# Kernel optimization log

Hardware: AMD Instinct MI355X
Metric: run time of the kernel (lower is better)

## Reference

```python
import jax, jax.numpy as jnp
import numpy as np
from jax import lax

B, T, D = 4, 4096, 1024  # d_inner == D (expansion=1.0)


def setup_inputs() -> dict:
    key = jax.random.key(0)
    ks = jax.random.split(key, 6)
    s = 1.0 / np.sqrt(D)  # xavier-ish scale
    return {
        "x": jax.random.normal(ks[0], (B, T, D), dtype=jnp.float32),
        "W_in": jax.random.normal(ks[1], (D, D), dtype=jnp.float32) * s,
        "W_alpha": jax.random.normal(ks[2], (D, D), dtype=jnp.float32) * s,
        "b_alpha": jnp.full((D,), 2.0, dtype=jnp.float32),
        "W_beta": jax.random.normal(ks[3], (D, D), dtype=jnp.float32) * s,
        "b_beta": jnp.zeros((D,), dtype=jnp.float32),
        "W_v": jax.random.normal(ks[4], (D, D), dtype=jnp.float32) * s,
        "b_v": jnp.zeros((D,), dtype=jnp.float32),
        "W_out": jax.random.normal(ks[5], (D, D), dtype=jnp.float32) * s,
    }


def reference(x, W_in, W_alpha, b_alpha, W_beta, b_beta, W_v, b_v, W_out):
    # x: [B, T, D]; torch nn.Linear convention y = x @ W.T
    xp = jax.nn.silu(jnp.einsum("btd,ed->bte", x, W_in))  # [B, T, Di]
    alpha = jax.nn.sigmoid(jnp.einsum("bte,fe->btf", xp, W_alpha) + b_alpha)
    beta = jax.nn.sigmoid(jnp.einsum("bte,fe->btf", xp, W_beta) + b_beta)
    v = jnp.tanh(jnp.einsum("bte,fe->btf", xp, W_v) + b_v)
    bv = beta * v  # precompute write term

    def step(h, ab):
        a_t, bv_t = ab  # each [B, Di]
        h = a_t * h + bv_t
        return h, h * jax.nn.silu(h)

    h0 = jnp.zeros((x.shape[0], W_alpha.shape[0]), dtype=x.dtype)
    h_last, outs = lax.scan(step, h0, (alpha.transpose(1, 0, 2), bv.transpose(1, 0, 2)))
    cell_out = outs.transpose(1, 0, 2)  # [B, T, Di]
    output = jnp.einsum("btf,df->btd", cell_out, W_out)
    return output, h_last
```

## Files before the change

### kernel.cpp

```cpp
#include <hip/hip_runtime.h>
#include <hip/hip_bf16.h>
#include <cstdint>
#include <cstddef>

typedef __bf16 bf16_t;
typedef _Float16 f16_t;
typedef __bf16 bf16x8 __attribute__((ext_vector_type(8)));
typedef float  f32x4  __attribute__((ext_vector_type(4)));

constexpr int kBatch = 4;
constexpr int kT = 4096;
constexpr int kD = 1024;
constexpr int kM = kBatch * kT;
constexpr int kCH = kBatch * kD;
constexpr int kNC = 128;
constexpr int kL  = kT / kNC;
constexpr int LDS_BYTES = 131072;

__device__ __forceinline__ void async16(const bf16_t* g, char* l) {
    __builtin_amdgcn_global_load_lds(
        (const __attribute__((address_space(1))) uint32_t*)g,
        (__attribute__((address_space(3))) uint32_t*)l,
        16, 0, 0);
}

__global__ void cvt_bf16_kernel(const float* __restrict__ in, bf16_t* __restrict__ out, int n8) {
    int i = blockIdx.x * blockDim.x + threadIdx.x;
    if (i >= n8) return;
    const float4* p = reinterpret_cast<const float4*>(in) + 2 * (size_t)i;
    float4 a = p[0], b = p[1];
    bf16x8 o;
    o[0] = (bf16_t)a.x; o[1] = (bf16_t)a.y; o[2] = (bf16_t)a.z; o[3] = (bf16_t)a.w;
    o[4] = (bf16_t)b.x; o[5] = (bf16_t)b.y; o[6] = (bf16_t)b.z; o[7] = (bf16_t)b.w;
    *reinterpret_cast<bf16x8*>(out + 8 * (size_t)i) = o;
}

__global__ void cvtw_kernel(const float* __restrict__ w0, const float* __restrict__ w1,
                            const float* __restrict__ w2, const float* __restrict__ w3,
                            const float* __restrict__ w4, bf16_t* __restrict__ out) {
    const int per = kD * kD / 8;
    int i = blockIdx.x * blockDim.x + threadIdx.x;
    int seg = i / per, j = i - seg * per;
    const float* src = seg == 0 ? w0 : seg == 1 ? w1 : seg == 2 ? w2 : seg == 3 ? w3 : w4;
    const float4* p = reinterpret_cast<const float4*>(src) + 2 * (size_t)j;
    float4 a = p[0], b = p[1];
    bf16x8 o;
    o[0] = (bf16_t)a.x; o[1] = (bf16_t)a.y; o[2] = (bf16_t)a.z; o[3] = (bf16_t)a.w;
    o[4] = (bf16_t)b.x; o[5] = (bf16_t)b.y; o[6] = (bf16_t)b.z; o[7] = (bf16_t)b.w;
    *reinterpret_cast<bf16x8*>(out + ((size_t)seg * per + j) * 8) = o;
}

template<int EPI>
__global__ __launch_bounds__(512, 2)
void gemm256(const bf16_t* __restrict__ A, const bf16_t* __restrict__ Bw,
             const float* __restrict__ bi0, const float* __restrict__ bi1,
             const float* __restrict__ bi2,
             void* __restrict__ out0, void* __restrict__ out1, void* __restrict__ out2,
             int M, int N, int K)
{
    extern __shared__ char lds[];
    const int tid  = threadIdx.x;
    const int lane = tid & 63;
    const int wv   = tid >> 6;
    const int wr   = wv >> 2;
    const int wc   = wv & 3;
    const int l16  = lane & 15;
    const int lhi  = lane >> 4;

    int bid = blockIdx.y * gridDim.x + blockIdx.x;
    int nwg = gridDim.x * gridDim.y;
    int swz = (bid & 7) * (nwg >> 3) + (bid >> 3);
    int gx  = N >> 8;
    int n0  = (swz % gx) << 8;
    int m0  = (swz / gx) << 8;

    auto goff = [&](int chunk) -> size_t {
        int st = chunk >> 6;
        int ri = (chunk >> 2) & 15;
        int cp = (chunk & 3) << 3;
        int cl = cp ^ (((ri >> 3) & 1) << 4);
        int gr = ((st >> 1) << 4) + ri;
        int gc = ((st & 1) << 5) + cl;
        return (size_t)gr * K + gc;
    };
    const size_t g0 = goff(tid), g1 = goff(512 + tid);
    const int d0 = wv << 10, d1 = 8192 + (wv << 10);

    auto STAGE = [&](const bf16_t* G, int row0, int k0, int lds_base) {
        const bf16_t* base = G + (size_t)row0 * K + k0;
        async16(base + g0, lds + lds_base + d0);
        async16(base + g1, lds + lds_base + d1);
    };
    auto STAGE_TILE = [&](int w, int bufo) {
        const int k0 = w << 6;
        STAGE(A,  m0,        k0, bufo);
        STAGE(A,  m0 + 128,  k0, bufo + 16384);
        STAGE(Bw, n0,        k0, bufo + 32768);
        STAGE(Bw, n0 + 128,  k0, bufo + 49152);
    };

    auto ldsoff = [&](int r, int c) -> int {
        int ri = r & 15;
        int st = ((r >> 4) << 1) | (c >> 5);
        int cw = (c & 31) ^ (((ri >> 3) & 1) << 4);
        return (st << 10) + (ri << 6) + (cw << 1);
    };
    int offA[4][2], offB[2][2];
#pragma unroll
    for (int m = 0; m < 4; ++m)
#pragma unroll
        for (int s = 0; s < 2; ++s)
            offA[m][s] = ldsoff(wr * 64 + m * 16 + l16, s * 32 + lhi * 8);
#pragma unroll
    for (int n = 0; n < 2; ++n)
#pragma unroll
        for (int s = 0; s < 2; ++s)
            offB[n][s] = ldsoff(wc * 32 + n * 16 + l16, s * 32 + lhi * 8);

    f32x4 acc[8][4];
#pragma unroll
    for (int i = 0; i < 8; ++i)
#pragma unroll
        for (int j = 0; j < 4; ++j)
            acc[i][j] = (f32x4){0.f, 0.f, 0.f, 0.f};

    const int NT = K >> 6;

    STAGE_TILE(0, 0);
    asm volatile("s_waitcnt vmcnt(0)" ::: "memory");
    asm volatile("s_barrier" ::: "memory");

    for (int w = 0; w < NT; ++w) {
        const int bufo  = (w & 1) << 16;
        const int nbufo = bufo ^ 65536;
        const int oA0 = bufo, oA1 = bufo + 16384;
        const int oB0 = bufo + 32768, oB1 = bufo + 49152;

        if (w + 1 < NT) STAGE_TILE(w + 1, nbufo);

#pragma unroll
        for (int s = 0; s < 2; ++s) {
            bf16x8 aL[4], aH[4], bL[2], bH[2];
#pragma unroll
            for (int m = 0; m < 4; ++m)
                aL[m] = *reinterpret_cast<const bf16x8*>(lds + oA0 + offA[m][s]);
#pragma unroll
            for (int n = 0; n < 2; ++n) {
                bL[n] = *reinterpret_cast<const bf16x8*>(lds + oB0 + offB[n][s]);
                bH[n] = *reinterpret_cast<const bf16x8*>(lds + oB1 + offB[n][s]);
            }
            __builtin_amdgcn_s_setprio(1);
#pragma unroll
            for (int m = 0; m < 4; ++m)
#pragma unroll
                for (int n = 0; n < 2; ++n) {
                    acc[m][n]     = __builtin_amdgcn_mfma_f32_16x16x32_bf16(aL[m], bL[n], acc[m][n], 0, 0, 0);
                    acc[m][2 + n] = __builtin_amdgcn_mfma_f32_16x16x32_bf16(aL[m], bH[n], acc[m][2 + n], 0, 0, 0);
                }
            __builtin_amdgcn_s_setprio(0);
#pragma unroll
            for (int m = 0; m < 4; ++m)
                aH[m] = *reinterpret_cast<const bf16x8*>(lds + oA1 + offA[m][s]);
            __builtin_amdgcn_s_setprio(1);
#pragma unroll
            for (int m = 0; m < 4; ++m)
#pragma unroll
                for (int n = 0; n < 2; ++n) {
                    acc[4 + m][n]     = __builtin_amdgcn_mfma_f32_16x16x32_bf16(aH[m], bL[n], acc[4 + m][n], 0, 0, 0);
                    acc[4 + m][2 + n] = __builtin_amdgcn_mfma_f32_16x16x32_bf16(aH[m], bH[n], acc[4 + m][2 + n], 0, 0, 0);
                }
            __builtin_amdgcn_s_setprio(0);
        }

        if (w + 1 < NT) {
            asm volatile("s_waitcnt vmcnt(0)" ::: "memory");
            asm volatile("s_barrier" ::: "memory");
        }
    }

    const int slab = n0 >> 10;
    const float* bia = (EPI == 4) ? (slab == 0 ? bi0 : slab == 1 ? bi1 : bi2) : nullptr;
#pragma unroll
    for (int j = 0; j < 4; ++j) {
        const int colg = n0 + ((j >> 1) << 7) + wc * 32 + (j & 1) * 16 + l16;
        const int cL = colg & (kD - 1);
        float bs = 0.f;
        if constexpr (EPI == 4) bs = bia[cL];
#pragma unroll
        for (int i = 0; i < 8; ++i) {
            const int rb = m0 + ((i >> 2) << 7) + wr * 64 + (i & 3) * 16 + lhi * 4;
#pragma unroll
            for (int r = 0; r < 4; ++r) {
                const int rowg = rb + r;
                const float f = acc[i][j][r];
                if constexpr (EPI == 0) {
                    float s = f / (1.f + __expf(-f));
                    reinterpret_cast<bf16_t*>(out0)[(size_t)rowg * N + colg] = (bf16_t)s;
                } else if constexpr (EPI == 3) {
                    __builtin_nontemporal_store(f, reinterpret_cast<float*>(out0) + (size_t)rowg * N + colg);
                } else {
                    const size_t idx = (size_t)rowg * kD + cL;
                    if (slab == 0) {
                        float s = 1.f / (1.f + __expf(-(f + bs)));
                        __builtin_nontemporal_store((f16_t)s, reinterpret_cast<f16_t*>(out0) + idx);
                    } else if (slab == 1) {
                        float s = 1.f / (1.f + __expf(-(f + bs)));
                        __builtin_nontemporal_store((bf16_t)s, reinterpret_cast<bf16_t*>(out1) + idx);
                    } else {
                        float s = tanhf(f + bs);
                        __builtin_nontemporal_store((bf16_t)s, reinterpret_cast<bf16_t*>(out2) + idx);
                    }
                }
            }
        }
    }
}

__global__ void scan_chunk_kernel(const f16_t* __restrict__ alpha,
                                  const bf16_t* __restrict__ beta,
                                  const bf16_t* __restrict__ vv,
                                  float* __restrict__ Aagg,
                                  float* __restrict__ Bagg)
{
    const int u  = blockIdx.x * blockDim.x + threadIdx.x;
    const int ch = u & (kCH - 1);
    const int c  = u >> 12;
    const int b  = ch >> 10;
    const int d  = ch & (kD - 1);
    size_t base = ((size_t)b * kT + (size_t)c * kL) * kD + d;
    float Ac = 1.f, Bc = 0.f;
#pragma unroll 4
    for (int t = 0; t < kL; ++t) {
        float a  = (float)alpha[base];
        float bv = (float)beta[base] * (float)vv[base];
        Ac *= a;
        Bc = a * Bc + bv;
        base += kD;
    }
    Aagg[u] = Ac;
    Bagg[u] = Bc;
}

__global__ void scan_mid_kernel(const float* __restrict__ Aagg,
                                const float* __restrict__ Bagg,
                                float* __restrict__ Hin,
                                float* __restrict__ hlast)
{
    const int ch = blockIdx.x * blockDim.x + threadIdx.x;
    float h = 0.f;
#pragma unroll 8
    for (int c = 0; c < kNC; ++c) {
        Hin[(size_t)c * kCH + ch] = h;
        h = Aagg[(size_t)c * kCH + ch] * h + Bagg[(size_t)c * kCH + ch];
    }
    hlast[ch] = h;
}

__global__ void scan_out_kernel(const f16_t* __restrict__ alpha,
                                const bf16_t* __restrict__ beta,
                                const bf16_t* __restrict__ vv,
                                const float* __restrict__ Hin,
                                bf16_t* __restrict__ cell)
{
    const int u  = blockIdx.x * blockDim.x + threadIdx.x;
    const int ch = u & (kCH - 1);
    const int c  = u >> 12;
    const int b  = ch >> 10;
    const int d  = ch & (kD - 1);
    size_t base = ((size_t)b * kT + (size_t)c * kL) * kD + d;
    float h = Hin[u];
#pragma unroll 4
    for (int t = 0; t < kL; ++t) {
        float a  = (float)alpha[base];
        float bv = (float)beta[base] * (float)vv[base];
        h = a * h + bv;
        float s = 1.f / (1.f + __expf(-h));
        cell[base] = (bf16_t)(h * h * s);
        base += kD;
    }
}

extern "C" void kernel_launch(void* const* d_in, const int* in_sizes, int n_in,
                              void* d_out, int out_size, void* d_ws, size_t ws_size,
                              hipStream_t stream)
{
    const float* x     = (const float*)d_in[0];
    const float* W_in  = (const float*)d_in[1];
    const float* W_al  = (const float*)d_in[2];
    const float* b_al  = (const float*)d_in[3];
    const float* W_be  = (const float*)d_in[4];
    const float* b_be  = (const float*)d_in[5];
    const float* W_v   = (const float*)d_in[6];
    const float* b_v   = (const float*)d_in[7];
    const float* W_out = (const float*)d_in[8];

    float* out   = (float*)d_out;
    float* hlast = out + (size_t)kM * kD;

    char* ws = (char*)d_ws;
    size_t off = 0;
    auto alloc = [&](size_t bytes) -> void* {
        void* p = ws + off;
        off += (bytes + 255) & ~(size_t)255;
        return p;
    };
    bf16_t* xbf   = (bf16_t*)alloc((size_t)kM * kD * 2);
    bf16_t* xp    = (bf16_t*)alloc((size_t)kM * kD * 2);
    f16_t*  alpha = (f16_t*) alloc((size_t)kM * kD * 2);
    bf16_t* betab = (bf16_t*)alloc((size_t)kM * kD * 2);
    bf16_t* vb    = (bf16_t*)alloc((size_t)kM * kD * 2);
    bf16_t* wbf   = (bf16_t*)alloc((size_t)5 * kD * kD * 2);

    bf16_t* Winb = wbf;
    bf16_t* Wfus = wbf + 1 * (size_t)kD * kD;
    bf16_t* Wob  = wbf + 4 * (size_t)kD * kD;

    bf16_t* cell = xbf;
    float*  Aagg = (float*)xp;
    float*  Bagg = Aagg + (size_t)kNC * kCH;
    float*  Hin  = Bagg + (size_t)kNC * kCH;

    hipFuncSetAttribute(reinterpret_cast<const void*>(gemm256<0>), hipFuncAttributeMaxDynamicSharedMemorySize, LDS_BYTES);
    hipFuncSetAttribute(reinterpret_cast<const void*>(gemm256<3>), hipFuncAttributeMaxDynamicSharedMemorySize, LDS_BYTES);
    hipFuncSetAttribute(reinterpret_cast<const void*>(gemm256<4>), hipFuncAttributeMaxDynamicSharedMemorySize, LDS_BYTES);

    {
        int n8 = kM * kD / 8;
        cvt_bf16_kernel<<<(n8 + 255) / 256, 256, 0, stream>>>(x, xbf, n8);
        int wtot = 5 * kD * kD / 8;
        cvtw_kernel<<<(wtot + 255) / 256, 256, 0, stream>>>(W_in, W_al, W_be, W_v, W_out, wbf);
    }

    dim3 grid1(kD / 256, kM / 256);
    dim3 gridF(3 * kD / 256, kM / 256);

    gemm256<0><<<grid1, 512, LDS_BYTES, stream>>>(xbf, Winb, nullptr, nullptr, nullptr,
                                                  xp, nullptr, nullptr, kM, kD, kD);
    gemm256<4><<<gridF, 512, LDS_BYTES, stream>>>(xp, Wfus, b_al, b_be, b_v,
                                                  alpha, betab, vb, kM, 3 * kD, kD);
    scan_chunk_kernel<<<kNC * kCH / 256, 256, 0, stream>>>(alpha, betab, vb, Aagg, Bagg);
    scan_mid_kernel<<<kCH / 256, 256, 0, stream>>>(Aagg, Bagg, Hin, hlast);
    scan_out_kernel<<<kNC * kCH / 256, 256, 0, stream>>>(alpha, betab, vb, Hin, cell);

    gemm256<3><<<grid1, 512, LDS_BYTES, stream>>>(cell, Wob, nullptr, nullptr, nullptr,
                                                  out, nullptr, nullptr, kM, kD, kD);
}
```

Measured before the change: 342.1 us.

## Loop fused GEMM over three N tiles per block, split staging, fast epilogue math

The fused alpha/beta/v GEMM now has each workgroup handle three consecutive 256-column tiles, so its grid shrinks from 768 to 256 blocks. Inside the K loop, the next tile's A and B loads are split and issued between the LDS fragment reads of the two k-substeps, and all four MFMA groups per substep are merged into one block. The epilogue replaces tanhf with a clamped exp-based tanh and uses a shared sigmoid helper. The aim is to cut tail/launch imbalance, overlap loads with compute better, and make the transcendental epilogue cheaper. The cost is fewer blocks to fill the CUs (256 blocks on 256 CUs) and a serialized re-prologue for each of the three tiles.

```diff
diff --git a/kernel.cpp b/kernel.cpp
--- a/kernel.cpp
+++ b/kernel.cpp
@@ -22,6 +22,15 @@
         (const __attribute__((address_space(1))) uint32_t*)g,
         (__attribute__((address_space(3))) uint32_t*)l,
         16, 0, 0);
+}
+
+__device__ __forceinline__ float fast_sigmoid(float z) {
+    return 1.f / (1.f + __expf(-z));
+}
+__device__ __forceinline__ float fast_tanh(float z) {
+    z = fminf(10.f, fmaxf(-10.f, z));
+    float e = __expf(2.f * z);
+    return (e - 1.f) / (e + 1.f);
 }
 
 __global__ void cvt_bf16_kernel(const float* __restrict__ in, bf16_t* __restrict__ out, int n8) {
@@ -50,7 +59,7 @@
     *reinterpret_cast<bf16x8*>(out + ((size_t)seg * per + j) * 8) = o;
 }
 
-template<int EPI>
+template<int EPI, int TPB>
 __global__ __launch_bounds__(512, 2)
 void gemm256(const bf16_t* __restrict__ A, const bf16_t* __restrict__ Bw,
              const float* __restrict__ bi0, const float* __restrict__ bi1,
@@ -70,8 +79,8 @@
     int bid = blockIdx.y * gridDim.x + blockIdx.x;
     int nwg = gridDim.x * gridDim.y;
     int swz = (bid & 7) * (nwg >> 3) + (bid >> 3);
-    int gx  = N >> 8;
-    int n0  = (swz % gx) << 8;
+    int gx  = (N >> 8) / TPB;
+    int nb0 = (swz % gx) * (TPB << 8);
     int m0  = (swz / gx) << 8;
 
     auto goff = [&](int chunk) -> size_t {
@@ -91,13 +100,6 @@
         async16(base + g0, lds + lds_base + d0);
         async16(base + g1, lds + lds_base + d1);
     };
-    auto STAGE_TILE = [&](int w, int bufo) {
-        const int k0 = w << 6;
-        STAGE(A,  m0,        k0, bufo);
-        STAGE(A,  m0 + 128,  k0, bufo + 16384);
-        STAGE(Bw, n0,        k0, bufo + 32768);
-        STAGE(Bw, n0 + 128,  k0, bufo + 49152);
-    };
 
     auto ldsoff = [&](int r, int c) -> int {
         int ri = r & 15;
@@ -117,98 +119,123 @@
         for (int s = 0; s < 2; ++s)
             offB[n][s] = ldsoff(wc * 32 + n * 16 + l16, s * 32 + lhi * 8);
 
-    f32x4 acc[8][4];
-#pragma unroll
-    for (int i = 0; i < 8; ++i)
-#pragma unroll
-        for (int j = 0; j < 4; ++j)
-            acc[i][j] = (f32x4){0.f, 0.f, 0.f, 0.f};
-
     const int NT = K >> 6;
 
-    STAGE_TILE(0, 0);
-    asm volatile("s_waitcnt vmcnt(0)" ::: "memory");
-    asm volatile("s_barrier" ::: "memory");
-
-    for (int w = 0; w < NT; ++w) {
-        const int bufo  = (w & 1) << 16;
-        const int nbufo = bufo ^ 65536;
-        const int oA0 = bufo, oA1 = bufo + 16384;
-        const int oB0 = bufo + 32768, oB1 = bufo + 49152;
-
-        if (w + 1 < NT) STAGE_TILE(w + 1, nbufo);
-
-#pragma unroll
-        for (int s = 0; s < 2; ++s) {
+    for (int it = 0; it < TPB; ++it) {
+        const int n0 = nb0 + (it << 8);
+
+        f32x4 acc[8][4];
+#pragma unroll
+        for (int i = 0; i < 8; ++i)
+#pragma unroll
+            for (int j = 0; j < 4; ++j)
+                acc[i][j] = (f32x4){0.f, 0.f, 0.f, 0.f};
+
+        STAGE(A,  m0,        0, 0);
+        STAGE(A,  m0 + 128,  0, 16384);
+        STAGE(Bw, n0,        0, 32768);
+        STAGE(Bw, n0 + 128,  0, 49152);
+        asm volatile("s_waitcnt vmcnt(0)" ::: "memory");
+        asm volatile("s_barrier" ::: "memory");
+
+        for (int w = 0; w < NT; ++w) {
+            const int bufo  = (w & 1) << 16;
+            const int nbufo = bufo ^ 65536;
+            const int oA0 = bufo, oA1 = bufo + 16384;
+            const int oB0 = bufo + 32768, oB1 = bufo + 49152;
+            const int k1 = (w + 1) << 6;
+
             bf16x8 aL[4], aH[4], bL[2], bH[2];
 #pragma unroll
+            for (int m = 0; m < 4; ++m) {
+                aL[m] = *reinterpret_cast<const bf16x8*>(lds + oA0 + offA[m][0]);
+                aH[m] = *reinterpret_cast<const bf16x8*>(lds + oA1 + offA[m][0]);
+            }
+#pragma unroll
+            for (int n = 0; n < 2; ++n) {
+                bL[n] = *reinterpret_cast<const bf16x8*>(lds + oB0 + offB[n][0]);
+                bH[n] = *reinterpret_cast<const bf16x8*>(lds + oB1 + offB[n][0]);
+            }
+            if (w + 1 < NT) {
+                STAGE(A, m0,       k1, nbufo);
+                STAGE(A, m0 + 128, k1, nbufo + 16384);
+            }
+            __builtin_amdgcn_s_setprio(1);
+#pragma unroll
             for (int m = 0; m < 4; ++m)
-                aL[m] = *reinterpret_cast<const bf16x8*>(lds + oA0 + offA[m][s]);
-#pragma unroll
-            for (int n = 0; n < 2; ++n) {
-                bL[n] = *reinterpret_cast<const bf16x8*>(lds + oB0 + offB[n][s]);
-                bH[n] = *reinterpret_cast<const bf16x8*>(lds + oB1 + offB[n][s]);
-            }
-            __builtin_amdgcn_s_setprio(1);
-#pragma unroll
-            for (int m = 0; m < 4; ++m)
 #pragma unroll
                 for (int n = 0; n < 2; ++n) {
-                    acc[m][n]     = __builtin_amdgcn_mfma_f32_16x16x32_bf16(aL[m], bL[n], acc[m][n], 0, 0, 0);
-                    acc[m][2 + n] = __builtin_amdgcn_mfma_f32_16x16x32_bf16(aL[m], bH[n], acc[m][2 + n], 0, 0, 0);
-                }
-            __builtin_amdgcn_s_setprio(0);
-#pragma unroll
-            for (int m = 0; m < 4; ++m)
-                aH[m] = *reinterpret_cast<const bf16x8*>(lds + oA1 + offA[m][s]);
-            __builtin_amdgcn_s_setprio(1);
-#pragma unroll
-            for (int m = 0; m < 4; ++m)
-#pragma unroll
-                for (int n = 0; n < 2; ++n) {
+                    acc[m][n]         = __builtin_amdgcn_mfma_f32_16x16x32_bf16(aL[m], bL[n], acc[m][n], 0, 0, 0);
+                    acc[m][2 + n]     = __builtin_amdgcn_mfma_f32_16x16x32_bf16(aL[m], bH[n], acc[m][2 + n], 0, 0, 0);
                     acc[4 + m][n]     = __builtin_amdgcn_mfma_f32_16x16x32_bf16(aH[m], bL[n], acc[4 + m][n], 0, 0, 0);
                     acc[4 + m][2 + n] = __builtin_amdgcn_mfma_f32_16x16x32_bf16(aH[m], bH[n], acc[4 + m][2 + n], 0, 0, 0);
                 }
             __builtin_amdgcn_s_setprio(0);
+
+#pragma unroll
+            for (int m = 0; m < 4; ++m) {
+                aL[m] = *reinterpret_cast<const bf16x8*>(lds + oA0 + offA[m][1]);
+                aH[m] = *reinterpret_cast<const bf16x8*>(lds + oA1 + offA[m][1]);
+            }
+#pragma unroll
+            for (int n = 0; n < 2; ++n) {
+                bL[n] = *reinterpret_cast<const bf16x8*>(lds + oB0 + offB[n][1]);
+                bH[n] = *reinterpret_cast<const bf16x8*>(lds + oB1 + offB[n][1]);
+            }
+            if (w + 1 < NT) {
+                STAGE(Bw, n0,       k1, nbufo + 32768);
+                STAGE(Bw, n0 + 128, k1, nbufo + 49152);
+            }
+            __builtin_amdgcn_s_setprio(1);
+#pragma unroll
+            for (int m = 0; m < 4; ++m)
+#pragma unroll
+                for (int n = 0; n < 2; ++n) {
+                    acc[m][n]         = __builtin_amdgcn_mfma_f32_16x16x32_bf16(aL[m], bL[n], acc[m][n], 0, 0, 0);
+                    acc[m][2 + n]     = __builtin_amdgcn_mfma_f32_16x16x32_bf16(aL[m], bH[n], acc[m][2 + n], 0, 0, 0);
+                    acc[4 + m][n]     = __builtin_amdgcn_mfma_f32_16x16x32_bf16(aH[m], bL[n], acc[4 + m][n], 0, 0, 0);
+                    acc[4 + m][2 + n] = __builtin_amdgcn_mfma_f32_16x16x32_bf16(aH[m], bH[n], acc[4 + m][2 + n], 0, 0, 0);
+                }
+            __builtin_amdgcn_s_setprio(0);
+
+            if (w + 1 < NT) {
+                asm volatile("s_waitcnt vmcnt(0)" ::: "memory");
+                asm volatile("s_barrier" ::: "memory");
+            }
         }
 
-        if (w + 1 < NT) {
-            asm volatile("s_waitcnt vmcnt(0)" ::: "memory");
-            asm volatile("s_barrier" ::: "memory");
-        }
-    }
-
-    const int slab = n0 >> 10;
-    const float* bia = (EPI == 4) ? (slab == 0 ? bi0 : slab == 1 ? bi1 : bi2) : nullptr;
-#pragma unroll
-    for (int j = 0; j < 4; ++j) {
-        const int colg = n0 + ((j >> 1) << 7) + wc * 32 + (j & 1) * 16 + l16;
-        const int cL = colg & (kD - 1);
-        float bs = 0.f;
-        if constexpr (EPI == 4) bs = bia[cL];
-#pragma unroll
-        for (int i = 0; i < 8; ++i) {
-            const int rb = m0 + ((i >> 2) << 7) + wr * 64 + (i & 3) * 16 + lhi * 4;
-#pragma unroll
-            for (int r = 0; r < 4; ++r) {
-                const int rowg = rb + r;
-                const float f = acc[i][j][r];
-                if constexpr (EPI == 0) {
-                    float s = f / (1.f + __expf(-f));
-                    reinterpret_cast<bf16_t*>(out0)[(size_t)rowg * N + colg] = (bf16_t)s;
-                } else if constexpr (EPI == 3) {
-                    __builtin_nontemporal_store(f, reinterpret_cast<float*>(out0) + (size_t)rowg * N + colg);
-                } else {
-                    const size_t idx = (size_t)rowg * kD + cL;
-                    if (slab == 0) {
-                        float s = 1.f / (1.f + __expf(-(f + bs)));
-                        __builtin_nontemporal_store((f16_t)s, reinterpret_cast<f16_t*>(out0) + idx);
-                    } else if (slab == 1) {
-                        float s = 1.f / (1.f + __expf(-(f + bs)));
-                        __builtin_nontemporal_store((bf16_t)s, reinterpret_cast<bf16_t*>(out1) + idx);
+        const int slab = n0 >> 10;
+        const float* bia = (EPI == 4) ? (slab == 0 ? bi0 : slab == 1 ? bi1 : bi2) : nullptr;
+#pragma unroll
+        for (int j = 0; j < 4; ++j) {
+            const int colg = n0 + ((j >> 1) << 7) + wc * 32 + (j & 1) * 16 + l16;
+            const int cL = colg & (kD - 1);
+            float bs = 0.f;
+            if constexpr (EPI == 4) bs = bia[cL];
+#pragma unroll
+            for (int i = 0; i < 8; ++i) {
+                const int rb = m0 + ((i >> 2) << 7) + wr * 64 + (i & 3) * 16 + lhi * 4;
+#pragma unroll
+                for (int r = 0; r < 4; ++r) {
+                    const int rowg = rb + r;
+                    const float f = acc[i][j][r];
+                    if constexpr (EPI == 0) {
+                        float s = f * fast_sigmoid(f);
+                        reinterpret_cast<bf16_t*>(out0)[(size_t)rowg * N + colg] = (bf16_t)s;
+                    } else if constexpr (EPI == 3) {
+                        __builtin_nontemporal_store(f, reinterpret_cast<float*>(out0) + (size_t)rowg * N + colg);
                     } else {
-                        float s = tanhf(f + bs);
-                        __builtin_nontemporal_store((bf16_t)s, reinterpret_cast<bf16_t*>(out2) + idx);
+                        const size_t idx = (size_t)rowg * kD + cL;
+                        if (slab == 0) {
+                            __builtin_nontemporal_store((f16_t)fast_sigmoid(f + bs),
+                                reinterpret_cast<f16_t*>(out0) + idx);
+                        } else if (slab == 1) {
+                            __builtin_nontemporal_store((bf16_t)fast_sigmoid(f + bs),
+                                reinterpret_cast<bf16_t*>(out1) + idx);
+                        } else {
+                            __builtin_nontemporal_store((bf16_t)fast_tanh(f + bs),
+                                reinterpret_cast<bf16_t*>(out2) + idx);
+                        }
                     }
                 }
             }
@@ -320,9 +347,9 @@
     float*  Bagg = Aagg + (size_t)kNC * kCH;
     float*  Hin  = Bagg + (size_t)kNC * kCH;
 
-    hipFuncSetAttribute(reinterpret_cast<const void*>(gemm256<0>), hipFuncAttributeMaxDynamicSharedMemorySize, LDS_BYTES);
-    hipFuncSetAttribute(reinterpret_cast<const void*>(gemm256<3>), hipFuncAttributeMaxDynamicSharedMemorySize, LDS_BYTES);
-    hipFuncSetAttribute(reinterpret_cast<const void*>(gemm256<4>), hipFuncAttributeMaxDynamicSharedMemorySize, LDS_BYTES);
+    hipFuncSetAttribute(reinterpret_cast<const void*>(gemm256<0,1>), hipFuncAttributeMaxDynamicSharedMemorySize, LDS_BYTES);
+    hipFuncSetAttribute(reinterpret_cast<const void*>(gemm256<3,1>), hipFuncAttributeMaxDynamicSharedMemorySize, LDS_BYTES);
+    hipFuncSetAttribute(reinterpret_cast<const void*>(gemm256<4,3>), hipFuncAttributeMaxDynamicSharedMemorySize, LDS_BYTES);
 
     {
         int n8 = kM * kD / 8;
@@ -332,16 +359,17 @@
     }
 
     dim3 grid1(kD / 256, kM / 256);
-    dim3 gridF(3 * kD / 256, kM / 256);
-
-    gemm256<0><<<grid1, 512, LDS_BYTES, stream>>>(xbf, Winb, nullptr, nullptr, nullptr,
-                                                  xp, nullptr, nullptr, kM, kD, kD);
-    gemm256<4><<<gridF, 512, LDS_BYTES, stream>>>(xp, Wfus, b_al, b_be, b_v,
-                                                  alpha, betab, vb, kM, 3 * kD, kD);
+    dim3 gridF(1, kM / 256);
+    gridF = dim3((3 * kD / 256) / 3, kM / 256);
+
+    gemm256<0,1><<<grid1, 512, LDS_BYTES, stream>>>(xbf, Winb, nullptr, nullptr, nullptr,
+                                                    xp, nullptr, nullptr, kM, kD, kD);
+    gemm256<4,3><<<gridF, 512, LDS_BYTES, stream>>>(xp, Wfus, b_al, b_be, b_v,
+                                                    alpha, betab, vb, kM, 3 * kD, kD);
     scan_chunk_kernel<<<kNC * kCH / 256, 256, 0, stream>>>(alpha, betab, vb, Aagg, Bagg);
     scan_mid_kernel<<<kCH / 256, 256, 0, stream>>>(Aagg, Bagg, Hin, hlast);
     scan_out_kernel<<<kNC * kCH / 256, 256, 0, stream>>>(alpha, betab, vb, Hin, cell);
 
-    gemm256<3><<<grid1, 512, LDS_BYTES, stream>>>(cell, Wob, nullptr, nullptr, nullptr,
-                                                  out, nullptr, nullptr, kM, kD, kD);
-}
+    gemm256<3,1><<<grid1, 512, LDS_BYTES, stream>>>(cell, Wob, nullptr, nullptr, nullptr,
+                                                    out, nullptr, nullptr, kM, kD, kD);
+}
```

Result: slower. 396.3 us (+15.8%).

## Switch GEMM to 32x32x16 MFMA with reorganized wave tiling and fast epilogue

Applied to the files above, without the earlier changes.

Replaces the 16x16x32 bf16 MFMA tiling with 32x32x16 MFMA instructions. Each wave now covers a 128x64 output sub-tile through new LDS fragment offsets and a new accumulator layout. The larger instruction does more work per operand read, which is meant to cut LDS reads and instruction issue per FLOP. The epilogue also swaps tanhf for an exp-based tanh and replaces the nontemporal half-precision stores with plain stores, which may change cache behaviour.

```diff
diff --git a/kernel.cpp b/kernel.cpp
--- a/kernel.cpp
+++ b/kernel.cpp
@@ -7,6 +7,7 @@
 typedef _Float16 f16_t;
 typedef __bf16 bf16x8 __attribute__((ext_vector_type(8)));
 typedef float  f32x4  __attribute__((ext_vector_type(4)));
+typedef float  f32x16 __attribute__((ext_vector_type(16)));
 
 constexpr int kBatch = 4;
 constexpr int kT = 4096;
@@ -22,6 +23,15 @@
         (const __attribute__((address_space(1))) uint32_t*)g,
         (__attribute__((address_space(3))) uint32_t*)l,
         16, 0, 0);
+}
+
+__device__ __forceinline__ float fast_sigmoid(float z) {
+    return 1.f / (1.f + __expf(-z));
+}
+__device__ __forceinline__ float fast_tanh(float z) {
+    z = fminf(10.f, fmaxf(-10.f, z));
+    float e = __expf(2.f * z);
+    return (e - 1.f) / (e + 1.f);
 }
 
 __global__ void cvt_bf16_kernel(const float* __restrict__ in, bf16_t* __restrict__ out, int n8) {
@@ -64,8 +74,8 @@
     const int wv   = tid >> 6;
     const int wr   = wv >> 2;
     const int wc   = wv & 3;
-    const int l16  = lane & 15;
-    const int lhi  = lane >> 4;
+    const int l32  = lane & 31;
+    const int lh   = lane >> 5;
 
     int bid = blockIdx.y * gridDim.x + blockIdx.x;
     int nwg = gridDim.x * gridDim.y;
@@ -105,24 +115,24 @@
         int cw = (c & 31) ^ (((ri >> 3) & 1) << 4);
         return (st << 10) + (ri << 6) + (cw << 1);
     };
-    int offA[4][2], offB[2][2];
+    int offA[4][4], offB[2][4];
 #pragma unroll
     for (int m = 0; m < 4; ++m)
 #pragma unroll
-        for (int s = 0; s < 2; ++s)
-            offA[m][s] = ldsoff(wr * 64 + m * 16 + l16, s * 32 + lhi * 8);
+        for (int ks = 0; ks < 4; ++ks)
+            offA[m][ks] = ldsoff(m * 32 + l32, ks * 16 + lh * 8);
 #pragma unroll
     for (int n = 0; n < 2; ++n)
 #pragma unroll
-        for (int s = 0; s < 2; ++s)
-            offB[n][s] = ldsoff(wc * 32 + n * 16 + l16, s * 32 + lhi * 8);
-
-    f32x4 acc[8][4];
-#pragma unroll
-    for (int i = 0; i < 8; ++i)
-#pragma unroll
-        for (int j = 0; j < 4; ++j)
-            acc[i][j] = (f32x4){0.f, 0.f, 0.f, 0.f};
+        for (int ks = 0; ks < 4; ++ks)
+            offB[n][ks] = ldsoff(((wc & 1) << 6) + n * 32 + l32, ks * 16 + lh * 8);
+
+    f32x16 acc[4][2];
+#pragma unroll
+    for (int i = 0; i < 4; ++i)
+#pragma unroll
+        for (int j = 0; j < 2; ++j)
+            acc[i][j] = (f32x16)(0.f);
 
     const int NT = K >> 6;
 
@@ -133,42 +143,26 @@
     for (int w = 0; w < NT; ++w) {
         const int bufo  = (w & 1) << 16;
         const int nbufo = bufo ^ 65536;
-        const int oA0 = bufo, oA1 = bufo + 16384;
-        const int oB0 = bufo + 32768, oB1 = bufo + 49152;
+        const int aReg = bufo + (wr << 14);
+        const int bReg = bufo + 32768 + ((wc >> 1) << 14);
 
         if (w + 1 < NT) STAGE_TILE(w + 1, nbufo);
 
 #pragma unroll
-        for (int s = 0; s < 2; ++s) {
-            bf16x8 aL[4], aH[4], bL[2], bH[2];
+        for (int ks = 0; ks < 4; ++ks) {
+            bf16x8 aF[4], bF[2];
 #pragma unroll
             for (int m = 0; m < 4; ++m)
-                aL[m] = *reinterpret_cast<const bf16x8*>(lds + oA0 + offA[m][s]);
-#pragma unroll
-            for (int n = 0; n < 2; ++n) {
-                bL[n] = *reinterpret_cast<const bf16x8*>(lds + oB0 + offB[n][s]);
-                bH[n] = *reinterpret_cast<const bf16x8*>(lds + oB1 + offB[n][s]);
-            }
+                aF[m] = *reinterpret_cast<const bf16x8*>(lds + aReg + offA[m][ks]);
+#pragma unroll
+            for (int n = 0; n < 2; ++n)
+                bF[n] = *reinterpret_cast<const bf16x8*>(lds + bReg + offB[n][ks]);
             __builtin_amdgcn_s_setprio(1);
 #pragma unroll
             for (int m = 0; m < 4; ++m)
 #pragma unroll
-                for (int n = 0; n < 2; ++n) {
-                    acc[m][n]     = __builtin_amdgcn_mfma_f32_16x16x32_bf16(aL[m], bL[n], acc[m][n], 0, 0, 0);
-                    acc[m][2 + n] = __builtin_amdgcn_mfma_f32_16x16x32_bf16(aL[m], bH[n], acc[m][2 + n], 0, 0, 0);
-                }
-            __builtin_amdgcn_s_setprio(0);
-#pragma unroll
-            for (int m = 0; m < 4; ++m)
-                aH[m] = *reinterpret_cast<const bf16x8*>(lds + oA1 + offA[m][s]);
-            __builtin_amdgcn_s_setprio(1);
-#pragma unroll
-            for (int m = 0; m < 4; ++m)
-#pragma unroll
-                for (int n = 0; n < 2; ++n) {
-                    acc[4 + m][n]     = __builtin_amdgcn_mfma_f32_16x16x32_bf16(aH[m], bL[n], acc[4 + m][n], 0, 0, 0);
-                    acc[4 + m][2 + n] = __builtin_amdgcn_mfma_f32_16x16x32_bf16(aH[m], bH[n], acc[4 + m][2 + n], 0, 0, 0);
-                }
+                for (int n = 0; n < 2; ++n)
+                    acc[m][n] = __builtin_amdgcn_mfma_f32_32x32x16_bf16(aF[m], bF[n], acc[m][n], 0, 0, 0);
             __builtin_amdgcn_s_setprio(0);
         }
 
@@ -181,34 +175,31 @@
     const int slab = n0 >> 10;
     const float* bia = (EPI == 4) ? (slab == 0 ? bi0 : slab == 1 ? bi1 : bi2) : nullptr;
 #pragma unroll
-    for (int j = 0; j < 4; ++j) {
-        const int colg = n0 + ((j >> 1) << 7) + wc * 32 + (j & 1) * 16 + l16;
+    for (int nf = 0; nf < 2; ++nf) {
+        const int colg = n0 + wc * 64 + nf * 32 + l32;
         const int cL = colg & (kD - 1);
         float bs = 0.f;
         if constexpr (EPI == 4) bs = bia[cL];
 #pragma unroll
-        for (int i = 0; i < 8; ++i) {
-            const int rb = m0 + ((i >> 2) << 7) + wr * 64 + (i & 3) * 16 + lhi * 4;
-#pragma unroll
-            for (int r = 0; r < 4; ++r) {
-                const int rowg = rb + r;
-                const float f = acc[i][j][r];
+        for (int mf = 0; mf < 4; ++mf) {
+            const int rbase = m0 + wr * 128 + mf * 32 + lh * 4;
+#pragma unroll
+            for (int rg = 0; rg < 16; ++rg) {
+                const int rowg = rbase + (rg & 3) + ((rg >> 2) << 3);
+                const float f = acc[mf][nf][rg];
                 if constexpr (EPI == 0) {
-                    float s = f / (1.f + __expf(-f));
+                    float s = f * fast_sigmoid(f);
                     reinterpret_cast<bf16_t*>(out0)[(size_t)rowg * N + colg] = (bf16_t)s;
                 } else if constexpr (EPI == 3) {
                     __builtin_nontemporal_store(f, reinterpret_cast<float*>(out0) + (size_t)rowg * N + colg);
                 } else {
                     const size_t idx = (size_t)rowg * kD + cL;
                     if (slab == 0) {
-                        float s = 1.f / (1.f + __expf(-(f + bs)));
-                        __builtin_nontemporal_store((f16_t)s, reinterpret_cast<f16_t*>(out0) + idx);
+                        reinterpret_cast<f16_t*>(out0)[idx] = (f16_t)fast_sigmoid(f + bs);
                     } else if (slab == 1) {
-                        float s = 1.f / (1.f + __expf(-(f + bs)));
-                        __builtin_nontemporal_store((bf16_t)s, reinterpret_cast<bf16_t*>(out1) + idx);
+                        reinterpret_cast<bf16_t*>(out1)[idx] = (bf16_t)fast_sigmoid(f + bs);
                     } else {
-                        float s = tanhf(f + bs);
-                        __builtin_nontemporal_store((bf16_t)s, reinterpret_cast<bf16_t*>(out2) + idx);
+                        reinterpret_cast<bf16_t*>(out2)[idx] = (bf16_t)fast_tanh(f + bs);
                     }
                 }
             }
```

Result: faster. 309.9 us (-9.4%).
